# Kernel tuning notes

Measured on AMD Instinct MI355X. Metric: run time of the kernel, lower is better.

Reference implementation:

```python
import jax, jax.numpy as jnp
import numpy as np

N = 100000   # num_nodes
F_IN = 128   # num_features
D = 64       # encoder_dim
E = 1600000  # num raw edges (avg degree 16)
BETA = 0.01  # perturb_value


def setup_inputs() -> dict:
    key = jax.random.key(0)
    ks = jax.random.split(key, 8)
    x = jax.random.normal(ks[0], (N, F_IN), dtype=jnp.float32)
    edge_index = jax.random.randint(ks[1], (2, E), 0, N, dtype=jnp.int64)
    W1 = jax.random.normal(ks[2], (F_IN, D), dtype=jnp.float32) * 0.05
    b1 = jnp.zeros((D,), dtype=jnp.float32)
    W2 = jax.random.normal(ks[3], (D, D), dtype=jnp.float32) * 0.05
    b2 = jnp.zeros((D,), dtype=jnp.float32)
    # torch FloatTensor(...).normal_(-beta, beta): mean=-beta, std=beta
    perturb1 = jax.random.normal(ks[4], (N, D), dtype=jnp.float32) * BETA - BETA
    perturb2 = jax.random.normal(ks[5], (N, D), dtype=jnp.float32) * BETA - BETA
    return {"x": x, "edge_index": edge_index, "W1": W1, "b1": b1,
            "W2": W2, "b2": b2, "perturb1": perturb1, "perturb2": perturb2}


def _graph_conv(h, src, dst, norm, W, b):
    # linear transform then gather -> weighted message -> scatter-add
    h = h @ W                                  # [N, D]
    msg = h[src] * norm[:, None]               # [E+N, D] irregular gather
    agg = jax.ops.segment_sum(msg, dst, num_segments=N)  # scatter-add
    return agg + b


def reference(x, edge_index, W1, b1, W2, b2, perturb1, perturb2):
    # add self-loops (GCN/PPMI-style propagation with symmetric norm;
    # PPMI edge weights approximated by degree normalization)
    loops = jnp.arange(N, dtype=edge_index.dtype)
    src = jnp.concatenate([edge_index[0], loops])
    dst = jnp.concatenate([edge_index[1], loops])
    deg = jax.ops.segment_sum(jnp.ones_like(dst, dtype=x.dtype), dst, num_segments=N)
    deg = jnp.maximum(deg, 1.0)
    norm = jax.lax.rsqrt(deg[src] * deg[dst])  # [E+N]

    h = _graph_conv(x, src, dst, norm, W1, b1) + perturb1
    h = jax.nn.relu(h)                         # dropout = identity (eval mode)
    h = _graph_conv(h, src, dst, norm, W2, b2) + perturb2
    return h
```

## Files before the change

kernel.cpp:

```cpp
#include <hip/hip_runtime.h>

#define DD 64
#define FIN 128
#define BK 256
#define MAXBUK 512
#define CAP 8192
#define ESCAP 12288
#define EPB 4096

typedef _Float16 half8 __attribute__((ext_vector_type(8)));
typedef float f32x4 __attribute__((ext_vector_type(4)));

static __device__ __forceinline__ void f16acc(uint4 v, float* a) {
    union { unsigned u; _Float16 h[2]; } t0, t1, t2, t3;
    t0.u = v.x; t1.u = v.y; t2.u = v.z; t3.u = v.w;
    a[0] += (float)t0.h[0]; a[1] += (float)t0.h[1];
    a[2] += (float)t1.h[0]; a[3] += (float)t1.h[1];
    a[4] += (float)t2.h[0]; a[5] += (float)t2.h[1];
    a[6] += (float)t3.h[0]; a[7] += (float)t3.h[1];
}

__global__ __launch_bounds__(256) void k_bucket(const int* __restrict__ src,
                                                const int* __restrict__ dst,
                                                unsigned* __restrict__ buf,
                                                int* __restrict__ gcur,
                                                int E, int nbuk) {
    __shared__ int hist[MAXBUK];
    __shared__ int base[MAXBUK];
    int e0 = blockIdx.x * EPB;
    int e1 = min(e0 + EPB, E);
    int dreg[16];
#pragma unroll
    for (int i = 0; i < 16; ++i) {
        int e = e0 + threadIdx.x + i * 256;
        dreg[i] = (e < e1) ? dst[e] : -1;
    }
    for (int i = threadIdx.x; i < nbuk; i += 256) hist[i] = 0;
    __syncthreads();
#pragma unroll
    for (int i = 0; i < 16; ++i)
        if (dreg[i] >= 0) atomicAdd(&hist[dreg[i] >> 8], 1);
    __syncthreads();
    for (int i = threadIdx.x; i < nbuk; i += 256) {
        int c = hist[i];
        base[i] = c ? atomicAdd(&gcur[i], c) : 0;
        hist[i] = 0;
    }
    __syncthreads();
#pragma unroll
    for (int i = 0; i < 16; ++i) {
        int d = dreg[i];
        if (d >= 0) {
            int e = e0 + threadIdx.x + i * 256;
            int b = d >> 8;
            int off = base[b] + atomicAdd(&hist[b], 1);
            if (off < CAP)
                buf[(size_t)b * CAP + off] = ((unsigned)src[e] << 8) | ((unsigned)d & 255u);
        }
    }
}

__global__ __launch_bounds__(256) void k_csr(const unsigned* __restrict__ buf,
                                             const int* __restrict__ gcur,
                                             int* __restrict__ rowptr,
                                             int* __restrict__ lenp,
                                             float* __restrict__ rs,
                                             int* __restrict__ es, int n, int dummy) {
    __shared__ int cnt[BK];
    __shared__ int excl[BK];
    __shared__ int cur[BK];
    __shared__ int wsum[4];
    int b = blockIdx.x;
    int tid = threadIdx.x;
    int lane = tid & 63, wid = tid >> 6;
    cnt[tid] = 0;
    cur[tid] = 0;
    __syncthreads();
    int count = gcur[b];
    const unsigned* rec = buf + (size_t)b * CAP;
    for (int i = tid; i < count; i += 256)
        atomicAdd(&cnt[rec[i] & (BK - 1)], 1);
    __syncthreads();
    int v = cnt[tid];
    int pv = (v + 15) & ~15;
    int s = pv;
    for (int off = 1; off < 64; off <<= 1) {
        int t = __shfl_up(s, off, 64);
        if (lane >= off) s += t;
    }
    if (lane == 63) wsum[wid] = s;
    __syncthreads();
    int wo = 0;
    for (int w = 0; w < wid; ++w) wo += wsum[w];
    excl[tid] = s - pv + wo;
    __syncthreads();
    int node = b * BK + tid;
    int base = b * ESCAP;
    if (node < n) {
        rowptr[node] = base + excl[tid];
        lenp[node] = pv;
        rs[node] = rsqrtf((float)(v + 1));
    }
    for (int i = tid; i < count; i += 256) {
        unsigned r = rec[i];
        int local = r & (BK - 1);
        int pos = base + excl[local] + atomicAdd(&cur[local], 1);
        es[pos] = (int)(r >> 8);
    }
    int st = base + excl[tid];
    for (int i = v; i < pv; ++i) es[st + i] = dummy;
}

__global__ __launch_bounds__(256) void k_prep(const float* __restrict__ W1,
                                              const float* __restrict__ W2,
                                              _Float16* __restrict__ Wt1,
                                              _Float16* __restrict__ Wt2) {
    int tid = threadIdx.x;
    for (int i = tid; i < FIN * DD; i += 256) {
        int k = i >> 6, c = i & 63;
        Wt1[c * FIN + k] = (_Float16)W1[i];
    }
    for (int i = tid; i < DD * DD; i += 256) {
        int k = i >> 6, c = i & 63;
        Wt2[c * DD + k] = (_Float16)W2[i];
    }
}

__global__ __launch_bounds__(256) void k_gemm1(const float* __restrict__ x,
                                               const _Float16* __restrict__ Wt,
                                               const float* __restrict__ rs,
                                               _Float16* __restrict__ hpf, int n) {
    __shared__ _Float16 sx[64 * 136];
    int row0 = blockIdx.x * 64;
    int tid = threadIdx.x;
    for (int i = tid; i < 2048; i += 256) {
        int r = i >> 5, c = i & 31;
        int row = row0 + r;
        float4 v = make_float4(0.f, 0.f, 0.f, 0.f);
        if (row < n) v = *(const float4*)(x + (size_t)row * FIN + c * 4);
        union { _Float16 h[4]; uint2 u; } t;
        t.h[0] = (_Float16)v.x; t.h[1] = (_Float16)v.y;
        t.h[2] = (_Float16)v.z; t.h[3] = (_Float16)v.w;
        *(uint2*)(sx + r * 136 + c * 4) = t.u;
    }
    __syncthreads();
    int lane = tid & 63, wave = tid >> 6;
    int r15 = lane & 15, g = lane >> 4;
    half8 a[4];
    const _Float16* ap = sx + (wave * 16 + r15) * 136 + g * 8;
#pragma unroll
    for (int kc = 0; kc < 4; ++kc) a[kc] = *(const half8*)(ap + kc * 32);
    half8 bfr[4][4];
    const _Float16* bp = Wt + (size_t)r15 * FIN + g * 8;
#pragma unroll
    for (int ct = 0; ct < 4; ++ct)
#pragma unroll
        for (int kc = 0; kc < 4; ++kc)
            bfr[ct][kc] = *(const half8*)(bp + ct * 16 * FIN + kc * 32);
    f32x4 acc[4] = {{0.f,0.f,0.f,0.f},{0.f,0.f,0.f,0.f},{0.f,0.f,0.f,0.f},{0.f,0.f,0.f,0.f}};
#pragma unroll
    for (int ct = 0; ct < 4; ++ct)
#pragma unroll
        for (int kc = 0; kc < 4; ++kc)
            acc[ct] = __builtin_amdgcn_mfma_f32_16x16x32_f16(a[kc], bfr[ct][kc], acc[ct], 0, 0, 0);
    __syncthreads();
#pragma unroll
    for (int reg = 0; reg < 4; ++reg) {
        int rowl = wave * 16 + g * 4 + reg;
        int row = row0 + rowl;
        float sc = (row < n) ? rs[row] : 0.f;
#pragma unroll
        for (int ct = 0; ct < 4; ++ct)
            sx[rowl * 72 + ct * 16 + r15] = (_Float16)(acc[ct][reg] * sc);
    }
    __syncthreads();
    for (int i = tid; i < 1024; i += 256) {
        int r = i >> 4, q = i & 15;
        uint2 v = *(const uint2*)(sx + r * 72 + q * 4);
        *(uint2*)(hpf + (size_t)(row0 + r) * DD + q * 4) = v;
    }
}

__global__ __launch_bounds__(256) void k_gemm2(const float* __restrict__ ain,
                                               const _Float16* __restrict__ Wt,
                                               const float* __restrict__ rs,
                                               _Float16* __restrict__ hpf, int n) {
    __shared__ _Float16 sx[64 * 72];
    int row0 = blockIdx.x * 64;
    int tid = threadIdx.x;
    for (int i = tid; i < 1024; i += 256) {
        int r = i >> 4, c = i & 15;
        int row = row0 + r;
        float4 v = make_float4(0.f, 0.f, 0.f, 0.f);
        if (row < n) {
            v = *(const float4*)(ain + (size_t)row * DD + c * 4);
            v.x = fmaxf(v.x, 0.f); v.y = fmaxf(v.y, 0.f);
            v.z = fmaxf(v.z, 0.f); v.w = fmaxf(v.w, 0.f);
        }
        union { _Float16 h[4]; uint2 u; } t;
        t.h[0] = (_Float16)v.x; t.h[1] = (_Float16)v.y;
        t.h[2] = (_Float16)v.z; t.h[3] = (_Float16)v.w;
        *(uint2*)(sx + r * 72 + c * 4) = t.u;
    }
    __syncthreads();
    int lane = tid & 63, wave = tid >> 6;
    int r15 = lane & 15, g = lane >> 4;
    half8 a[2];
    const _Float16* ap = sx + (wave * 16 + r15) * 72 + g * 8;
#pragma unroll
    for (int kc = 0; kc < 2; ++kc) a[kc] = *(const half8*)(ap + kc * 32);
    half8 bfr[4][2];
    const _Float16* bp = Wt + (size_t)r15 * DD + g * 8;
#pragma unroll
    for (int ct = 0; ct < 4; ++ct)
#pragma unroll
        for (int kc = 0; kc < 2; ++kc)
            bfr[ct][kc] = *(const half8*)(bp + ct * 16 * DD + kc * 32);
    f32x4 acc[4] = {{0.f,0.f,0.f,0.f},{0.f,0.f,0.f,0.f},{0.f,0.f,0.f,0.f},{0.f,0.f,0.f,0.f}};
#pragma unroll
    for (int ct = 0; ct < 4; ++ct)
#pragma unroll
        for (int kc = 0; kc < 2; ++kc)
            acc[ct] = __builtin_amdgcn_mfma_f32_16x16x32_f16(a[kc], bfr[ct][kc], acc[ct], 0, 0, 0);
    __syncthreads();
#pragma unroll
    for (int reg = 0; reg < 4; ++reg) {
        int rowl = wave * 16 + g * 4 + reg;
        int row = row0 + rowl;
        float sc = (row < n) ? rs[row] : 0.f;
#pragma unroll
        for (int ct = 0; ct < 4; ++ct)
            sx[rowl * 72 + ct * 16 + r15] = (_Float16)(acc[ct][reg] * sc);
    }
    __syncthreads();
    for (int i = tid; i < 1024; i += 256) {
        int r = i >> 4, q = i & 15;
        uint2 v = *(const uint2*)(sx + r * 72 + q * 4);
        *(uint2*)(hpf + (size_t)(row0 + r) * DD + q * 4) = v;
    }
}

__global__ __launch_bounds__(256) void k_agg(const uint4* __restrict__ hp4,
                                             const int* __restrict__ es,
                                             const int* __restrict__ rowptr,
                                             const int* __restrict__ lenp,
                                             const float* __restrict__ rs,
                                             const float* __restrict__ b,
                                             const float* __restrict__ pert,
                                             float* __restrict__ outp, int n) {
    int lane = threadIdx.x & 63;
    int wv = threadIdx.x >> 6;
    int g = lane >> 4;
    int sub = lane & 15;
    int eslot = sub >> 3;
    int q = sub & 7;
    int node = (blockIdx.x * 4 + wv) * 4 + g;
    bool alive = node < n;
    int nc = alive ? node : 0;
    int e0 = rowptr[nc];
    int len = alive ? lenp[nc] : 0;
    float A[8] = {0,0,0,0,0,0,0,0};
    float B[8] = {0,0,0,0,0,0,0,0};
    float C[8] = {0,0,0,0,0,0,0,0};
    float D[8] = {0,0,0,0,0,0,0,0};
    if (alive && eslot == 0) f16acc(hp4[(size_t)nc * 8 + q], A);
    for (int eb = e0; eb < e0 + len; eb += 16) {
        int idx = es[eb + sub];
        int i0 = __shfl(idx, 0 + eslot, 16);
        int i1 = __shfl(idx, 2 + eslot, 16);
        int i2 = __shfl(idx, 4 + eslot, 16);
        int i3 = __shfl(idx, 6 + eslot, 16);
        int i4 = __shfl(idx, 8 + eslot, 16);
        int i5 = __shfl(idx, 10 + eslot, 16);
        int i6 = __shfl(idx, 12 + eslot, 16);
        int i7 = __shfl(idx, 14 + eslot, 16);
        uint4 v0 = hp4[(size_t)i0 * 8 + q];
        uint4 v1 = hp4[(size_t)i1 * 8 + q];
        uint4 v2 = hp4[(size_t)i2 * 8 + q];
        uint4 v3 = hp4[(size_t)i3 * 8 + q];
        uint4 v4 = hp4[(size_t)i4 * 8 + q];
        uint4 v5 = hp4[(size_t)i5 * 8 + q];
        uint4 v6 = hp4[(size_t)i6 * 8 + q];
        uint4 v7 = hp4[(size_t)i7 * 8 + q];
        f16acc(v0, A); f16acc(v1, B); f16acc(v2, C); f16acc(v3, D);
        f16acc(v4, A); f16acc(v5, B); f16acc(v6, C); f16acc(v7, D);
    }
#pragma unroll
    for (int j = 0; j < 8; ++j) {
        float v = (A[j] + B[j]) + (C[j] + D[j]);
        v += __shfl_xor(v, 8, 64);
        A[j] = v;
    }
    if (alive && eslot == 0) {
        float r = rs[nc];
        size_t o = (size_t)nc * DD + q * 8;
        float4 p0 = *(const float4*)(pert + o);
        float4 p1 = *(const float4*)(pert + o + 4);
        float4 b0 = *(const float4*)(b + q * 8);
        float4 b1 = *(const float4*)(b + q * 8 + 4);
        float4 r0, r1;
        r0.x = fmaf(r, A[0], b0.x + p0.x);
        r0.y = fmaf(r, A[1], b0.y + p0.y);
        r0.z = fmaf(r, A[2], b0.z + p0.z);
        r0.w = fmaf(r, A[3], b0.w + p0.w);
        r1.x = fmaf(r, A[4], b1.x + p1.x);
        r1.y = fmaf(r, A[5], b1.y + p1.y);
        r1.z = fmaf(r, A[6], b1.z + p1.z);
        r1.w = fmaf(r, A[7], b1.w + p1.w);
        *(float4*)(outp + o) = r0;
        *(float4*)(outp + o + 4) = r1;
    }
}

extern "C" void kernel_launch(void* const* d_in, const int* in_sizes, int n_in,
                              void* d_out, int out_size, void* d_ws, size_t ws_size,
                              hipStream_t stream) {
    const float* x  = (const float*)d_in[0];
    const int*   ei = (const int*)d_in[1];
    const float* W1 = (const float*)d_in[2];
    const float* b1 = (const float*)d_in[3];
    const float* W2 = (const float*)d_in[4];
    const float* b2 = (const float*)d_in[5];
    const float* p1 = (const float*)d_in[6];
    const float* p2 = (const float*)d_in[7];
    float* out = (float*)d_out;

    int n = in_sizes[0] / FIN;
    int E = in_sizes[1] / 2;
    const int* src = ei;
    const int* dst = ei + E;
    int nbuk = (n + BK - 1) / BK;
    int gb = (n + 63) / 64;

    char* ws = (char*)d_ws;
    size_t off = 0;
    int* gcur   = (int*)(ws + off); off += sizeof(int) * MAXBUK;
    int* rowptr = (int*)(ws + off); off += sizeof(int) * (size_t)n;
    int* lenp   = (int*)(ws + off); off += sizeof(int) * (size_t)n;
    float* rs   = (float*)(ws + off); off += sizeof(float) * (size_t)n;
    int* es     = (int*)(ws + off); off += sizeof(int) * (size_t)nbuk * ESCAP;
    off = (off + 15) & ~(size_t)15;
    unsigned* buf = (unsigned*)(ws + off);
    off += sizeof(unsigned) * (size_t)nbuk * CAP;
    off = (off + 15) & ~(size_t)15;
    _Float16* hpf = (_Float16*)(ws + off);
    off += (size_t)gb * 64 * DD * 2;
    off = (off + 15) & ~(size_t)15;
    _Float16* Wt1 = (_Float16*)(ws + off); off += FIN * DD * 2;
    _Float16* Wt2 = (_Float16*)(ws + off); off += DD * DD * 2;
    off = (off + 15) & ~(size_t)15;
    float* agg1 = (float*)(ws + off); off += sizeof(float) * (size_t)n * DD;

    int ab = (n + 15) / 16;
    int bb = (E + EPB - 1) / EPB;

    hipMemsetAsync(gcur, 0, sizeof(int) * MAXBUK, stream);
    k_prep<<<1, 256, 0, stream>>>(W1, W2, Wt1, Wt2);
    k_bucket<<<bb, 256, 0, stream>>>(src, dst, buf, gcur, E, nbuk);
    k_csr<<<nbuk, 256, 0, stream>>>(buf, gcur, rowptr, lenp, rs, es, n, n);

    k_gemm1<<<gb, 256, 0, stream>>>(x, Wt1, rs, hpf, n);
    k_agg<<<ab, 256, 0, stream>>>((const uint4*)hpf, es, rowptr, lenp, rs, b1, p1, agg1, n);

    k_gemm2<<<gb, 256, 0, stream>>>(agg1, Wt2, rs, hpf, n);
    k_agg<<<ab, 256, 0, stream>>>((const uint4*)hpf, es, rowptr, lenp, rs, b2, p2, out, n);
}
```

Before: 168.6 us.

## Fuse layer-1 aggregation with layer-2 GEMM and accumulate gathers in packed fp16

Merges the first aggregation kernel with the second GEMM. The aggregated, ReLU'd rows go straight into shared memory as fp16 and feed the MFMA, so the fp32 agg1 intermediate is never written or re-read. The gather is reorganised so 4 lanes cover one node with 16-edge batches loaded as uint4. Accumulation now uses packed half2 adds instead of fp32 converts. It also folds the gcur memset into k_prep to drop one launch. The fp16 accumulation over up to ~16+ neighbours may lose precision, and fewer lanes per node with bigger unrolls raises register pressure.

```diff
diff --git a/kernel.cpp b/kernel.cpp
--- a/kernel.cpp
+++ b/kernel.cpp
@@ -9,16 +9,10 @@
 #define EPB 4096
 
 typedef _Float16 half8 __attribute__((ext_vector_type(8)));
+typedef _Float16 h2 __attribute__((ext_vector_type(2)));
 typedef float f32x4 __attribute__((ext_vector_type(4)));
 
-static __device__ __forceinline__ void f16acc(uint4 v, float* a) {
-    union { unsigned u; _Float16 h[2]; } t0, t1, t2, t3;
-    t0.u = v.x; t1.u = v.y; t2.u = v.z; t3.u = v.w;
-    a[0] += (float)t0.h[0]; a[1] += (float)t0.h[1];
-    a[2] += (float)t1.h[0]; a[3] += (float)t1.h[1];
-    a[4] += (float)t2.h[0]; a[5] += (float)t2.h[1];
-    a[6] += (float)t3.h[0]; a[7] += (float)t3.h[1];
-}
+union U4 { uint4 u; h2 h[4]; };
 
 __global__ __launch_bounds__(256) void k_bucket(const int* __restrict__ src,
                                                 const int* __restrict__ dst,
@@ -114,8 +108,11 @@
 __global__ __launch_bounds__(256) void k_prep(const float* __restrict__ W1,
                                               const float* __restrict__ W2,
                                               _Float16* __restrict__ Wt1,
-                                              _Float16* __restrict__ Wt2) {
+                                              _Float16* __restrict__ Wt2,
+                                              int* __restrict__ gcur) {
     int tid = threadIdx.x;
+    gcur[tid] = 0;
+    gcur[tid + 256] = 0;
     for (int i = tid; i < FIN * DD; i += 256) {
         int k = i >> 6, c = i & 63;
         Wt1[c * FIN + k] = (_Float16)W1[i];
@@ -181,36 +178,115 @@
     }
 }
 
-__global__ __launch_bounds__(256) void k_gemm2(const float* __restrict__ ain,
-                                               const _Float16* __restrict__ Wt,
-                                               const float* __restrict__ rs,
-                                               _Float16* __restrict__ hpf, int n) {
+#define GATHER_BODY                                                              \
+    int e0 = rowptr[nc];                                                         \
+    int len = alive ? lenp[nc] : 0;                                              \
+    int nbt = len >> 4;                                                          \
+    h2 ac[2][2][4] = {};                                                         \
+    {                                                                            \
+        U4 t0, t1;                                                               \
+        t0.u = hp4[(size_t)nc * 8 + q];                                          \
+        t1.u = hp4[(size_t)nc * 8 + q + 4];                                      \
+        _Pragma("unroll")                                                        \
+        for (int k = 0; k < 4; ++k) { ac[0][0][k] += t0.h[k]; ac[1][0][k] += t1.h[k]; } \
+    }                                                                            \
+    for (int t = 0; t < nbt; ++t) {                                              \
+        uint4 eb = *(const uint4*)(es + e0 + t * 16 + q * 4);                    \
+        int jj[16];                                                              \
+        _Pragma("unroll")                                                        \
+        for (int l = 0; l < 4; ++l) {                                            \
+            jj[l]      = __shfl((int)eb.x, l, 4);                                \
+            jj[4 + l]  = __shfl((int)eb.y, l, 4);                                \
+            jj[8 + l]  = __shfl((int)eb.z, l, 4);                                \
+            jj[12 + l] = __shfl((int)eb.w, l, 4);                                \
+        }                                                                        \
+        _Pragma("unroll")                                                        \
+        for (int hb = 0; hb < 2; ++hb) {                                         \
+            U4 v0[8], v1[8];                                                     \
+            _Pragma("unroll")                                                    \
+            for (int m = 0; m < 8; ++m) {                                        \
+                size_t bb = (size_t)jj[hb * 8 + m] * 8;                          \
+                v0[m].u = hp4[bb + q];                                           \
+                v1[m].u = hp4[bb + q + 4];                                       \
+            }                                                                    \
+            _Pragma("unroll")                                                    \
+            for (int m = 0; m < 8; ++m) {                                        \
+                _Pragma("unroll")                                                \
+                for (int k = 0; k < 4; ++k) {                                    \
+                    ac[0][m & 1][k] += v0[m].h[k];                               \
+                    ac[1][m & 1][k] += v1[m].h[k];                               \
+                }                                                                \
+            }                                                                    \
+        }                                                                        \
+    }                                                                            \
+    float F0[8], F1[8];                                                          \
+    _Pragma("unroll")                                                            \
+    for (int k = 0; k < 4; ++k) {                                                \
+        F0[2 * k]     = (float)ac[0][0][k].x + (float)ac[0][1][k].x;             \
+        F0[2 * k + 1] = (float)ac[0][0][k].y + (float)ac[0][1][k].y;             \
+        F1[2 * k]     = (float)ac[1][0][k].x + (float)ac[1][1][k].x;             \
+        F1[2 * k + 1] = (float)ac[1][0][k].y + (float)ac[1][1][k].y;             \
+    }
+
+__global__ __launch_bounds__(256) void k_aggemm(const uint4* __restrict__ hp4,
+                                                const int* __restrict__ es,
+                                                const int* __restrict__ rowptr,
+                                                const int* __restrict__ lenp,
+                                                const float* __restrict__ rs,
+                                                const float* __restrict__ b,
+                                                const float* __restrict__ pert,
+                                                const _Float16* __restrict__ Wt,
+                                                _Float16* __restrict__ hpo, int n) {
     __shared__ _Float16 sx[64 * 72];
+    int tid = threadIdx.x;
+    int lane = tid & 63, wv = tid >> 6;
+    int q = lane & 3, g = lane >> 2;
     int row0 = blockIdx.x * 64;
-    int tid = threadIdx.x;
-    for (int i = tid; i < 1024; i += 256) {
-        int r = i >> 4, c = i & 15;
-        int row = row0 + r;
-        float4 v = make_float4(0.f, 0.f, 0.f, 0.f);
-        if (row < n) {
-            v = *(const float4*)(ain + (size_t)row * DD + c * 4);
-            v.x = fmaxf(v.x, 0.f); v.y = fmaxf(v.y, 0.f);
-            v.z = fmaxf(v.z, 0.f); v.w = fmaxf(v.w, 0.f);
-        }
-        union { _Float16 h[4]; uint2 u; } t;
-        t.h[0] = (_Float16)v.x; t.h[1] = (_Float16)v.y;
-        t.h[2] = (_Float16)v.z; t.h[3] = (_Float16)v.w;
-        *(uint2*)(sx + r * 72 + c * 4) = t.u;
-    }
-    __syncthreads();
-    int lane = tid & 63, wave = tid >> 6;
-    int r15 = lane & 15, g = lane >> 4;
+    int rowl = wv * 16 + g;
+    int node = row0 + rowl;
+    bool alive = node < n;
+    int nc = alive ? node : 0;
+    GATHER_BODY
+    {
+        float r = rs[nc];
+        size_t op = (size_t)nc * DD + q * 8;
+        float4 p0 = *(const float4*)(pert + op);
+        float4 p1 = *(const float4*)(pert + op + 4);
+        float4 p2 = *(const float4*)(pert + op + 32);
+        float4 p3 = *(const float4*)(pert + op + 36);
+        float4 b0 = *(const float4*)(b + q * 8);
+        float4 b1 = *(const float4*)(b + q * 8 + 4);
+        float4 b2 = *(const float4*)(b + q * 8 + 32);
+        float4 b3 = *(const float4*)(b + q * 8 + 36);
+        union { _Float16 h[8]; uint4 u; } t0, t1;
+        float m = alive ? 1.f : 0.f;
+        t0.h[0] = (_Float16)(m * fmaxf(fmaf(r, F0[0], b0.x + p0.x), 0.f));
+        t0.h[1] = (_Float16)(m * fmaxf(fmaf(r, F0[1], b0.y + p0.y), 0.f));
+        t0.h[2] = (_Float16)(m * fmaxf(fmaf(r, F0[2], b0.z + p0.z), 0.f));
+        t0.h[3] = (_Float16)(m * fmaxf(fmaf(r, F0[3], b0.w + p0.w), 0.f));
+        t0.h[4] = (_Float16)(m * fmaxf(fmaf(r, F0[4], b1.x + p1.x), 0.f));
+        t0.h[5] = (_Float16)(m * fmaxf(fmaf(r, F0[5], b1.y + p1.y), 0.f));
+        t0.h[6] = (_Float16)(m * fmaxf(fmaf(r, F0[6], b1.z + p1.z), 0.f));
+        t0.h[7] = (_Float16)(m * fmaxf(fmaf(r, F0[7], b1.w + p1.w), 0.f));
+        t1.h[0] = (_Float16)(m * fmaxf(fmaf(r, F1[0], b2.x + p2.x), 0.f));
+        t1.h[1] = (_Float16)(m * fmaxf(fmaf(r, F1[1], b2.y + p2.y), 0.f));
+        t1.h[2] = (_Float16)(m * fmaxf(fmaf(r, F1[2], b2.z + p2.z), 0.f));
+        t1.h[3] = (_Float16)(m * fmaxf(fmaf(r, F1[3], b2.w + p2.w), 0.f));
+        t1.h[4] = (_Float16)(m * fmaxf(fmaf(r, F1[4], b3.x + p3.x), 0.f));
+        t1.h[5] = (_Float16)(m * fmaxf(fmaf(r, F1[5], b3.y + p3.y), 0.f));
+        t1.h[6] = (_Float16)(m * fmaxf(fmaf(r, F1[6], b3.z + p3.z), 0.f));
+        t1.h[7] = (_Float16)(m * fmaxf(fmaf(r, F1[7], b3.w + p3.w), 0.f));
+        *(uint4*)(sx + rowl * 72 + q * 8) = t0.u;
+        *(uint4*)(sx + rowl * 72 + q * 8 + 32) = t1.u;
+    }
+    __syncthreads();
+    int r15 = lane & 15, gg = lane >> 4;
     half8 a[2];
-    const _Float16* ap = sx + (wave * 16 + r15) * 72 + g * 8;
+    const _Float16* ap = sx + (wv * 16 + r15) * 72 + gg * 8;
 #pragma unroll
     for (int kc = 0; kc < 2; ++kc) a[kc] = *(const half8*)(ap + kc * 32);
     half8 bfr[4][2];
-    const _Float16* bp = Wt + (size_t)r15 * DD + g * 8;
+    const _Float16* bp = Wt + (size_t)r15 * DD + gg * 8;
 #pragma unroll
     for (int ct = 0; ct < 4; ++ct)
 #pragma unroll
@@ -225,90 +301,68 @@
     __syncthreads();
 #pragma unroll
     for (int reg = 0; reg < 4; ++reg) {
-        int rowl = wave * 16 + g * 4 + reg;
-        int row = row0 + rowl;
+        int rl = wv * 16 + gg * 4 + reg;
+        int row = row0 + rl;
         float sc = (row < n) ? rs[row] : 0.f;
 #pragma unroll
         for (int ct = 0; ct < 4; ++ct)
-            sx[rowl * 72 + ct * 16 + r15] = (_Float16)(acc[ct][reg] * sc);
+            sx[rl * 72 + ct * 16 + r15] = (_Float16)(acc[ct][reg] * sc);
     }
     __syncthreads();
     for (int i = tid; i < 1024; i += 256) {
-        int r = i >> 4, q = i & 15;
-        uint2 v = *(const uint2*)(sx + r * 72 + q * 4);
-        *(uint2*)(hpf + (size_t)(row0 + r) * DD + q * 4) = v;
-    }
-}
-
-__global__ __launch_bounds__(256) void k_agg(const uint4* __restrict__ hp4,
-                                             const int* __restrict__ es,
-                                             const int* __restrict__ rowptr,
-                                             const int* __restrict__ lenp,
-                                             const float* __restrict__ rs,
-                                             const float* __restrict__ b,
-                                             const float* __restrict__ pert,
-                                             float* __restrict__ outp, int n) {
-    int lane = threadIdx.x & 63;
-    int wv = threadIdx.x >> 6;
-    int g = lane >> 4;
-    int sub = lane & 15;
-    int eslot = sub >> 3;
-    int q = sub & 7;
-    int node = (blockIdx.x * 4 + wv) * 4 + g;
+        int r = i >> 4, qq = i & 15;
+        uint2 v = *(const uint2*)(sx + r * 72 + qq * 4);
+        *(uint2*)(hpo + (size_t)(row0 + r) * DD + qq * 4) = v;
+    }
+}
+
+__global__ __launch_bounds__(256) void k_agg2(const uint4* __restrict__ hp4,
+                                              const int* __restrict__ es,
+                                              const int* __restrict__ rowptr,
+                                              const int* __restrict__ lenp,
+                                              const float* __restrict__ rs,
+                                              const float* __restrict__ b,
+                                              const float* __restrict__ pert,
+                                              float* __restrict__ outp, int n) {
+    int tid = threadIdx.x;
+    int lane = tid & 63, wv = tid >> 6;
+    int q = lane & 3, g = lane >> 2;
+    int node = blockIdx.x * 64 + wv * 16 + g;
     bool alive = node < n;
     int nc = alive ? node : 0;
-    int e0 = rowptr[nc];
-    int len = alive ? lenp[nc] : 0;
-    float A[8] = {0,0,0,0,0,0,0,0};
-    float B[8] = {0,0,0,0,0,0,0,0};
-    float C[8] = {0,0,0,0,0,0,0,0};
-    float D[8] = {0,0,0,0,0,0,0,0};
-    if (alive && eslot == 0) f16acc(hp4[(size_t)nc * 8 + q], A);
-    for (int eb = e0; eb < e0 + len; eb += 16) {
-        int idx = es[eb + sub];
-        int i0 = __shfl(idx, 0 + eslot, 16);
-        int i1 = __shfl(idx, 2 + eslot, 16);
-        int i2 = __shfl(idx, 4 + eslot, 16);
-        int i3 = __shfl(idx, 6 + eslot, 16);
-        int i4 = __shfl(idx, 8 + eslot, 16);
-        int i5 = __shfl(idx, 10 + eslot, 16);
-        int i6 = __shfl(idx, 12 + eslot, 16);
-        int i7 = __shfl(idx, 14 + eslot, 16);
-        uint4 v0 = hp4[(size_t)i0 * 8 + q];
-        uint4 v1 = hp4[(size_t)i1 * 8 + q];
-        uint4 v2 = hp4[(size_t)i2 * 8 + q];
-        uint4 v3 = hp4[(size_t)i3 * 8 + q];
-        uint4 v4 = hp4[(size_t)i4 * 8 + q];
-        uint4 v5 = hp4[(size_t)i5 * 8 + q];
-        uint4 v6 = hp4[(size_t)i6 * 8 + q];
-        uint4 v7 = hp4[(size_t)i7 * 8 + q];
-        f16acc(v0, A); f16acc(v1, B); f16acc(v2, C); f16acc(v3, D);
-        f16acc(v4, A); f16acc(v5, B); f16acc(v6, C); f16acc(v7, D);
-    }
-#pragma unroll
-    for (int j = 0; j < 8; ++j) {
-        float v = (A[j] + B[j]) + (C[j] + D[j]);
-        v += __shfl_xor(v, 8, 64);
-        A[j] = v;
-    }
-    if (alive && eslot == 0) {
+    GATHER_BODY
+    if (alive) {
         float r = rs[nc];
-        size_t o = (size_t)nc * DD + q * 8;
-        float4 p0 = *(const float4*)(pert + o);
-        float4 p1 = *(const float4*)(pert + o + 4);
+        size_t op = (size_t)nc * DD + q * 8;
+        float4 p0 = *(const float4*)(pert + op);
+        float4 p1 = *(const float4*)(pert + op + 4);
+        float4 p2 = *(const float4*)(pert + op + 32);
+        float4 p3 = *(const float4*)(pert + op + 36);
         float4 b0 = *(const float4*)(b + q * 8);
         float4 b1 = *(const float4*)(b + q * 8 + 4);
-        float4 r0, r1;
-        r0.x = fmaf(r, A[0], b0.x + p0.x);
-        r0.y = fmaf(r, A[1], b0.y + p0.y);
-        r0.z = fmaf(r, A[2], b0.z + p0.z);
-        r0.w = fmaf(r, A[3], b0.w + p0.w);
-        r1.x = fmaf(r, A[4], b1.x + p1.x);
-        r1.y = fmaf(r, A[5], b1.y + p1.y);
-        r1.z = fmaf(r, A[6], b1.z + p1.z);
-        r1.w = fmaf(r, A[7], b1.w + p1.w);
-        *(float4*)(outp + o) = r0;
-        *(float4*)(outp + o + 4) = r1;
+        float4 b2 = *(const float4*)(b + q * 8 + 32);
+        float4 b3 = *(const float4*)(b + q * 8 + 36);
+        float4 r0, r1, r2, r3;
+        r0.x = fmaf(r, F0[0], b0.x + p0.x);
+        r0.y = fmaf(r, F0[1], b0.y + p0.y);
+        r0.z = fmaf(r, F0[2], b0.z + p0.z);
+        r0.w = fmaf(r, F0[3], b0.w + p0.w);
+        r1.x = fmaf(r, F0[4], b1.x + p1.x);
+        r1.y = fmaf(r, F0[5], b1.y + p1.y);
+        r1.z = fmaf(r, F0[6], b1.z + p1.z);
+        r1.w = fmaf(r, F0[7], b1.w + p1.w);
+        r2.x = fmaf(r, F1[0], b2.x + p2.x);
+        r2.y = fmaf(r, F1[1], b2.y + p2.y);
+        r2.z = fmaf(r, F1[2], b2.z + p2.z);
+        r2.w = fmaf(r, F1[3], b2.w + p2.w);
+        r3.x = fmaf(r, F1[4], b3.x + p3.x);
+        r3.y = fmaf(r, F1[5], b3.y + p3.y);
+        r3.z = fmaf(r, F1[6], b3.z + p3.z);
+        r3.w = fmaf(r, F1[7], b3.w + p3.w);
+        *(float4*)(outp + op) = r0;
+        *(float4*)(outp + op + 4) = r1;
+        *(float4*)(outp + op + 32) = r2;
+        *(float4*)(outp + op + 36) = r3;
     }
 }
 
@@ -330,7 +384,7 @@
     const int* src = ei;
     const int* dst = ei + E;
     int nbuk = (n + BK - 1) / BK;
-    int gb = (n + 63) / 64;
+    int gb = (n + 64) / 64;
 
     char* ws = (char*)d_ws;
     size_t off = 0;
@@ -346,22 +400,22 @@
     _Float16* hpf = (_Float16*)(ws + off);
     off += (size_t)gb * 64 * DD * 2;
     off = (off + 15) & ~(size_t)15;
+    _Float16* hp2 = (_Float16*)(ws + off);
+    off += (size_t)gb * 64 * DD * 2;
+    off = (off + 15) & ~(size_t)15;
     _Float16* Wt1 = (_Float16*)(ws + off); off += FIN * DD * 2;
     _Float16* Wt2 = (_Float16*)(ws + off); off += DD * DD * 2;
-    off = (off + 15) & ~(size_t)15;
-    float* agg1 = (float*)(ws + off); off += sizeof(float) * (size_t)n * DD;
-
-    int ab = (n + 15) / 16;
+
     int bb = (E + EPB - 1) / EPB;
-
-    hipMemsetAsync(gcur, 0, sizeof(int) * MAXBUK, stream);
-    k_prep<<<1, 256, 0, stream>>>(W1, W2, Wt1, Wt2);
+    int ab = (n + 63) / 64;
+
+    k_prep<<<1, 256, 0, stream>>>(W1, W2, Wt1, Wt2, gcur);
     k_bucket<<<bb, 256, 0, stream>>>(src, dst, buf, gcur, E, nbuk);
     k_csr<<<nbuk, 256, 0, stream>>>(buf, gcur, rowptr, lenp, rs, es, n, n);
 
     k_gemm1<<<gb, 256, 0, stream>>>(x, Wt1, rs, hpf, n);
-    k_agg<<<ab, 256, 0, stream>>>((const uint4*)hpf, es, rowptr, lenp, rs, b1, p1, agg1, n);
-
-    k_gemm2<<<gb, 256, 0, stream>>>(agg1, Wt2, rs, hpf, n);
-    k_agg<<<ab, 256, 0, stream>>>((const uint4*)hpf, es, rowptr, lenp, rs, b2, p2, out, n);
-}
+    k_aggemm<<<gb, 256, 0, stream>>>((const uint4*)hpf, es, rowptr, lenp, rs,
+                                     b1, p1, Wt2, hp2, n);
+    k_agg2<<<ab, 256, 0, stream>>>((const uint4*)hp2, es, rowptr, lenp, rs,
+                                   b2, p2, out, n);
+}
```

Result: faster. 153.5 us, median of 2 (-9.0%).
